# Optimization experiments

Hardware: AMD Instinct MI355X
Metric: run time of the kernel (lower is better)

Reference implementation:

```python
import jax, jax.numpy as jnp
import numpy as np

B, S, K_IN = 8, 2048, 512
D_MODEL = 1024
N_INPUT = 2048
N_PROCESS = 4096
HIDDEN = 4096  # default hidden_dim = n_input * 2
K = 256


def setup_inputs() -> dict:
    key = jax.random.key(0)
    ks = jax.random.split(key, 7)
    return {
        "selected_activations": jax.random.normal(ks[0], (B, S, K_IN), dtype=jnp.float32),
        "selected_indices": jax.random.randint(ks[1], (B, K_IN), 0, N_INPUT),
        "k": K,
        "combination_weights": jax.random.normal(ks[2], (N_PROCESS, N_INPUT), dtype=jnp.float32) * np.float32(np.sqrt(2.0 / N_INPUT)),
        "output_projections": jax.random.normal(ks[3], (N_PROCESS, D_MODEL), dtype=jnp.float32) * np.float32(np.sqrt(2.0 / N_PROCESS)),
        "w1": jax.random.normal(ks[4], (HIDDEN, N_INPUT), dtype=jnp.float32) * np.float32(np.sqrt(2.0 / (N_INPUT + HIDDEN))),
        "b1": jnp.zeros((HIDDEN,), dtype=jnp.float32),
        "w2": jax.random.normal(ks[5], (N_PROCESS, HIDDEN), dtype=jnp.float32) * np.float32(np.sqrt(2.0 / (HIDDEN + N_PROCESS))),
        "b2": jnp.zeros((N_PROCESS,), dtype=jnp.float32),
    }


def reference(selected_activations, selected_indices, k, combination_weights,
              output_projections, w1, b1, w2, b2):
    bsz = selected_indices.shape[0]
    n_input = combination_weights.shape[1]

    # Per-batch gather of combination weights: [B, k_in, n_process]
    sel_w = combination_weights.T[selected_indices]

    # Process activations: [B, S, n_process], exact (erf) GELU like torch F.gelu
    process_activations = jax.nn.gelu(
        jnp.einsum('bsk,bkp->bsp', selected_activations, sel_w), approximate=False)

    # One-hot style input-selection mask via scatter: [B, n_input]
    input_selection = jnp.zeros((bsz, n_input), dtype=jnp.float32)
    input_selection = input_selection.at[jnp.arange(bsz)[:, None], selected_indices].set(1.0)

    # Combination analyzer MLP: Linear -> GELU -> Linear
    h = jax.nn.gelu(input_selection @ w1.T + b1, approximate=False)
    combination_relevance = h @ w2.T + b2  # [B, n_process]

    # Router scores and top-k process selection
    activation_scores = process_activations.max(axis=1)  # [B, n_process]
    final_scores = activation_scores * jax.nn.sigmoid(combination_relevance)
    _, process_indices = jax.lax.top_k(final_scores, k)  # [B, k]

    # Gather selected process activations [B, S, k] and projections [B, k, d_model]
    sel_pa = jnp.take_along_axis(process_activations, process_indices[:, None, :], axis=2)
    sel_proj = output_projections[process_indices]

    # Final projection: [B, S, d_model]
    return jnp.einsum('bsk,bkd->bsd', sel_pa, sel_proj)
```

## Files before the change

kernel.cpp:

```cpp
#include <hip/hip_runtime.h>
#include <math.h>

#define B 8
#define S 2048
#define KIN 512
#define NIN 2048
#define NP 4096
#define HID 4096
#define DM 1024
#define TOPK 256

typedef __bf16 bf16x8 __attribute__((ext_vector_type(8)));
typedef __bf16 bf16x4 __attribute__((ext_vector_type(4)));
typedef float f32x4 __attribute__((ext_vector_type(4)));

__device__ __forceinline__ float gelu_exact(float x) {
    return 0.5f * x * (1.0f + erff(x * 0.70710678118654752440f));
}

__device__ __forceinline__ void atomicMaxFloat(float* addr, float val) {
    if (val >= 0.0f) atomicMax((int*)addr, __float_as_int(val));
    else             atomicMin((unsigned int*)addr, __float_as_uint(val));
}

__device__ __forceinline__ void async_copy16(void* lds, const void* g) {
    __builtin_amdgcn_global_load_lds(
        (__attribute__((address_space(1))) void*)g,
        (__attribute__((address_space(3))) void*)lds, 16, 0, 0);
}

__global__ __launch_bounds__(256) void init_kernel(float* scores, float* relacc,
                                                   float* hacc, unsigned* maskb,
                                                   int* selcnt) {
    int t = blockIdx.x * blockDim.x + threadIdx.x;
    if (t < B * NP)  { scores[t] = __int_as_float(0xFF800000); relacc[t] = 0.f; }
    if (t < B * HID) hacc[t] = 0.f;
    if (t < NIN)     maskb[t] = 0u;
    if (t < B)       selcnt[t] = 0;
}

__global__ __launch_bounds__(256) void scatter_maskbits(const int* __restrict__ idx,
                                                        unsigned* __restrict__ maskb) {
    int t = blockIdx.x * blockDim.x + threadIdx.x;
    if (t >= B * KIN) return;
    int b = t / KIN;
    atomicOr(&maskb[idx[t]], 1u << b);
}

__global__ __launch_bounds__(256) void pack_A(const float* __restrict__ A,
                                              __bf16* __restrict__ Apack) {
    size_t t = (size_t)blockIdx.x * 256 + threadIdx.x;
    size_t f = t * 4;
    size_t rowi = f >> 9;
    int j = (int)(f & 511);
    float4 v = *(const float4*)(A + f);
    __bf16 h0 = (__bf16)v.x, h1 = (__bf16)v.y, h2 = (__bf16)v.z, h3 = (__bf16)v.w;
    bf16x4 hv = {h0, h1, h2, h3};
    bf16x4 lv = {(__bf16)(v.x - (float)h0), (__bf16)(v.y - (float)h1),
                 (__bf16)(v.z - (float)h2), (__bf16)(v.w - (float)h3)};
    __bf16* orow = Apack + rowi * 1024;
    *(bf16x4*)(orow + j) = hv;
    *(bf16x4*)(orow + 512 + j) = lv;
}

__global__ __launch_bounds__(256) void gather_pack_w(const float* __restrict__ cw,
                                                     const int* __restrict__ idx,
                                                     __bf16* __restrict__ wpack) {
    __shared__ float rowbuf[4][NIN];
    __shared__ int sidx[B][KIN];
    int p0 = blockIdx.x * 4;
    int tid = threadIdx.x;
    for (int t = tid; t < B * KIN; t += 256) sidx[t >> 9][t & 511] = idx[t];
#pragma unroll
    for (int r = 0; r < 4; ++r)
        for (int c = tid; c < NIN / 4; c += 256)
            *(float4*)&rowbuf[r][c * 4] = *(const float4*)&cw[(size_t)(p0 + r) * NIN + c * 4];
    __syncthreads();
#pragma unroll
    for (int r = 0; r < 4; ++r) {
        int p = p0 + r;
        for (int b = 0; b < B; ++b) {
            __bf16* orow = wpack + ((size_t)b * NP + p) * 1024;
            for (int j = tid; j < KIN; j += 256) {
                float x = rowbuf[r][sidx[b][j]];
                __bf16 hh = (__bf16)x;
                orow[j] = hh;
                orow[512 + j] = (__bf16)(x - (float)hh);
            }
        }
    }
}

template <int EPI, int NSEG, int KSEG, int LDA, int LDB, int BROWS, int LDOUT>
__global__ __launch_bounds__(256) void mfma_gemm(const __bf16* __restrict__ Ap,
                                                 const __bf16* __restrict__ Bp,
                                                 void* __restrict__ outp) {
    __shared__ __align__(16) __bf16 As[128 * 64];
    __shared__ __align__(16) __bf16 Ws[128 * 64];
    const int b = blockIdx.z;
    const int s0 = blockIdx.x * 128;
    const int p0 = blockIdx.y * 128;
    const int tid = threadIdx.x;
    const int w = tid >> 6, lane = tid & 63;
    const int wr = w >> 1, wc = w & 1;
    const int ldRow = lane >> 3;
    const int ldCol = ((lane & 7) ^ (ldRow & 7)) * 8;
    const int fr = lane & 15;
    const int fq = lane >> 4;
    const __bf16* Ab = Ap + ((size_t)b * S + s0) * LDA;
    const __bf16* Bb = Bp + ((size_t)b * BROWS + p0) * LDB;

    f32x4 acc[4][4] = {};

    for (int seg = 0; seg < NSEG; ++seg) {
        const int aoff = (seg == 1) ? KSEG : 0;
        const int boff = (seg == 2) ? KSEG : 0;
        for (int k0 = 0; k0 < KSEG; k0 += 64) {
            __syncthreads();
#pragma unroll
            for (int i = 0; i < 4; ++i) {
                const __bf16* g = Ab + (size_t)(w * 32 + i * 8 + ldRow) * LDA + aoff + k0 + ldCol;
                async_copy16(&As[(w * 32 + i * 8) * 64], g);
            }
#pragma unroll
            for (int i = 0; i < 4; ++i) {
                const __bf16* g = Bb + (size_t)(w * 32 + i * 8 + ldRow) * LDB + boff + k0 + ldCol;
                async_copy16(&Ws[(w * 32 + i * 8) * 64], g);
            }
            __syncthreads();
#pragma unroll
            for (int ks = 0; ks < 2; ++ks) {
                bf16x8 af[4], bfr[4];
#pragma unroll
                for (int i = 0; i < 4; ++i) {
                    int R = wr * 64 + i * 16 + fr;
                    af[i] = *(const bf16x8*)&As[R * 64 + (((ks * 4 + fq) ^ (R & 7)) * 8)];
                }
#pragma unroll
                for (int j = 0; j < 4; ++j) {
                    int R = wc * 64 + j * 16 + fr;
                    bfr[j] = *(const bf16x8*)&Ws[R * 64 + (((ks * 4 + fq) ^ (R & 7)) * 8)];
                }
#pragma unroll
                for (int i = 0; i < 4; ++i)
#pragma unroll
                    for (int j = 0; j < 4; ++j)
                        acc[i][j] = __builtin_amdgcn_mfma_f32_16x16x32_bf16(af[i], bfr[j], acc[i][j], 0, 0, 0);
            }
        }
    }

    if constexpr (EPI == 1) {
        __bf16* o = (__bf16*)outp;
#pragma unroll
        for (int i = 0; i < 4; ++i)
#pragma unroll
            for (int r = 0; r < 4; ++r) {
                size_t row = (size_t)b * S + s0 + wr * 64 + i * 16 + fq * 4 + r;
#pragma unroll
                for (int j = 0; j < 4; ++j)
                    o[row * LDOUT + p0 + wc * 64 + j * 16 + fr] = (__bf16)gelu_exact(acc[i][j][r]);
            }
    } else {
        float* o = (float*)outp;
#pragma unroll
        for (int i = 0; i < 4; ++i)
#pragma unroll
            for (int r = 0; r < 4; ++r) {
                size_t row = (size_t)b * S + s0 + wr * 64 + i * 16 + fq * 4 + r;
#pragma unroll
                for (int j = 0; j < 4; ++j)
                    o[row * LDOUT + p0 + wc * 64 + j * 16 + fr] = acc[i][j][r];
            }
    }
}

__device__ __forceinline__ void stage64(__bf16* ldsTile, const __bf16* gRow0,
                                        int rbase, int ldg, int koff, int w, int lane) {
    const int rr = lane >> 3;
    const int gc = ((lane & 7) ^ rr) * 8;
    const __bf16* g = gRow0 + (size_t)(rbase + w * 8 + rr) * ldg + (koff + gc);
    async_copy16(ldsTile + (rbase + w * 8) * 64, g);
}

__device__ __forceinline__ void read_frags4(const __bf16* base, int row0, int fr,
                                            int fq, int kk, bf16x8* f) {
#pragma unroll
    for (int i = 0; i < 4; ++i) {
        int R = row0 + i * 16 + fr;
        f[i] = *(const bf16x8*)&base[R * 64 + (((kk * 4 + fq) ^ (R & 7)) * 8)];
    }
}

template <int EPI, int NSEG, int KSEG, int LDA, int LDB, int BROWS, int LDOUT>
__global__ __launch_bounds__(512, 2) void mfma_gemm256(const __bf16* __restrict__ Ap,
                                                       const __bf16* __restrict__ Bp,
                                                       void* __restrict__ outp) {
    constexpr int TPS = KSEG / 64;
    constexpr int NT = NSEG * TPS;
    __shared__ __align__(16) __bf16 As[2][256 * 64];
    __shared__ __align__(16) __bf16 Ws[2][256 * 64];
    const int b = blockIdx.z;
    const int s0 = blockIdx.x * 256;
    const int p0 = blockIdx.y * 256;
    const int tid = threadIdx.x;
    const int w = tid >> 6, lane = tid & 63;
    const int wr = w >> 2, wc = w & 3;
    const int fr = lane & 15, fq = lane >> 4;
    const __bf16* Ab = Ap + ((size_t)b * S + s0) * LDA;
    const __bf16* Bb = Bp + ((size_t)b * BROWS + p0) * LDB;

    auto offs = [&](int t, int& ao, int& bo) {
        int seg = t / TPS, k0 = (t % TPS) * 64;
        ao = ((NSEG == 3 && seg == 1) ? KSEG : 0) + k0;
        bo = ((NSEG == 3 && seg == 2) ? KSEG : 0) + k0;
    };

    f32x4 acc[8][4] = {};

    {
        int ao, bo;
        offs(0, ao, bo);
        stage64(&As[0][0], Ab, 0, LDA, ao, w, lane);
        stage64(&As[0][0], Ab, 128, LDA, ao, w, lane);
        stage64(&As[0][0], Ab, 64, LDA, ao, w, lane);
        stage64(&As[0][0], Ab, 192, LDA, ao, w, lane);
        stage64(&Ws[0][0], Bb, 0, LDB, bo, w, lane);
        stage64(&Ws[0][0], Bb, 128, LDB, bo, w, lane);
        stage64(&Ws[0][0], Bb, 64, LDB, bo, w, lane);
        stage64(&Ws[0][0], Bb, 192, LDB, bo, w, lane);
        if (NT > 1) {
            offs(1, ao, bo);
            stage64(&As[1][0], Ab, 0, LDA, ao, w, lane);
            stage64(&As[1][0], Ab, 128, LDA, ao, w, lane);
            stage64(&Ws[1][0], Bb, 0, LDB, bo, w, lane);
            stage64(&Ws[1][0], Bb, 128, LDB, bo, w, lane);
            asm volatile("s_waitcnt vmcnt(4)");
        } else {
            asm volatile("s_waitcnt vmcnt(0)");
        }
        __builtin_amdgcn_s_barrier();
    }

    for (int t = 0; t < NT; ++t) {
        __bf16* Asb = &As[t & 1][0];
        __bf16* Wsb = &Ws[t & 1][0];
        __bf16* Asn = &As[(t & 1) ^ 1][0];
        __bf16* Wsn = &Ws[(t & 1) ^ 1][0];
        bf16x8 af[4], bfr[4];

        read_frags4(Asb, wr * 128, fr, fq, 0, af);
        read_frags4(Wsb, wc * 64, fr, fq, 0, bfr);
        if (t + 1 < NT) {
            int ao, bo;
            offs(t + 1, ao, bo);
            stage64(Asn, Ab, 64, LDA, ao, w, lane);
            stage64(Asn, Ab, 192, LDA, ao, w, lane);
            stage64(Wsn, Bb, 64, LDB, bo, w, lane);
            stage64(Wsn, Bb, 192, LDB, bo, w, lane);
        }
        __builtin_amdgcn_s_barrier();
        asm volatile("s_waitcnt lgkmcnt(0)");
        __builtin_amdgcn_s_setprio(1);
#pragma unroll
        for (int mi = 0; mi < 4; ++mi)
#pragma unroll
            for (int nj = 0; nj < 4; ++nj)
                acc[mi][nj] = __builtin_amdgcn_mfma_f32_16x16x32_bf16(af[mi], bfr[nj], acc[mi][nj], 0, 0, 0);
        __builtin_amdgcn_s_setprio(0);
        __builtin_amdgcn_s_barrier();

        read_frags4(Asb, wr * 128 + 64, fr, fq, 0, af);
        __builtin_amdgcn_s_barrier();
        asm volatile("s_waitcnt lgkmcnt(0)");
        __builtin_amdgcn_s_setprio(1);
#pragma unroll
        for (int mi = 0; mi < 4; ++mi)
#pragma unroll
            for (int nj = 0; nj < 4; ++nj)
                acc[4 + mi][nj] = __builtin_amdgcn_mfma_f32_16x16x32_bf16(af[mi], bfr[nj], acc[4 + mi][nj], 0, 0, 0);
        __builtin_amdgcn_s_setprio(0);
        __builtin_amdgcn_s_barrier();

        read_frags4(Asb, wr * 128, fr, fq, 1, af);
        read_frags4(Wsb, wc * 64, fr, fq, 1, bfr);
        __builtin_amdgcn_s_barrier();
        asm volatile("s_waitcnt lgkmcnt(0)");
        __builtin_amdgcn_s_setprio(1);
#pragma unroll
        for (int mi = 0; mi < 4; ++mi)
#pragma unroll
            for (int nj = 0; nj < 4; ++nj)
                acc[mi][nj] = __builtin_amdgcn_mfma_f32_16x16x32_bf16(af[mi], bfr[nj], acc[mi][nj], 0, 0, 0);
        __builtin_amdgcn_s_setprio(0);
        __builtin_amdgcn_s_barrier();

        read_frags4(Asb, wr * 128 + 64, fr, fq, 1, af);
        if (t + 2 < NT) {
            int ao, bo;
            offs(t + 2, ao, bo);
            stage64(Asb, Ab, 0, LDA, ao, w, lane);
            stage64(Asb, Ab, 128, LDA, ao, w, lane);
            stage64(Wsb, Bb, 0, LDB, bo, w, lane);
            stage64(Wsb, Bb, 128, LDB, bo, w, lane);
            asm volatile("s_waitcnt vmcnt(4)");
        } else {
            asm volatile("s_waitcnt vmcnt(0)");
        }
        __builtin_amdgcn_s_barrier();
        asm volatile("s_waitcnt lgkmcnt(0)");
        __builtin_amdgcn_s_setprio(1);
#pragma unroll
        for (int mi = 0; mi < 4; ++mi)
#pragma unroll
            for (int nj = 0; nj < 4; ++nj)
                acc[4 + mi][nj] = __builtin_amdgcn_mfma_f32_16x16x32_bf16(af[mi], bfr[nj], acc[4 + mi][nj], 0, 0, 0);
        __builtin_amdgcn_s_setprio(0);
        __builtin_amdgcn_s_barrier();
    }

    if constexpr (EPI == 0) {
        float* scores = (float*)outp;
#pragma unroll
        for (int nj = 0; nj < 4; ++nj) {
            float mx = -INFINITY, mn = INFINITY;
#pragma unroll
            for (int mi = 0; mi < 8; ++mi)
#pragma unroll
                for (int r = 0; r < 4; ++r) {
                    float v = acc[mi][nj][r];
                    mx = fmaxf(mx, v);
                    mn = fminf(mn, v);
                }
            mx = fmaxf(mx, __shfl_xor(mx, 16));
            mx = fmaxf(mx, __shfl_xor(mx, 32));
            mn = fminf(mn, __shfl_xor(mn, 16));
            mn = fminf(mn, __shfl_xor(mn, 32));
            if (fq == 0) {
                float m = fmaxf(gelu_exact(mx), gelu_exact(mn));
                atomicMaxFloat(&scores[(size_t)b * LDOUT + p0 + wc * 64 + nj * 16 + fr], m);
            }
        }
    } else if constexpr (EPI == 1) {
        __bf16* o = (__bf16*)outp;
#pragma unroll
        for (int mi = 0; mi < 8; ++mi)
#pragma unroll
            for (int r = 0; r < 4; ++r) {
                size_t row = (size_t)b * S + s0 + wr * 128 + mi * 16 + fq * 4 + r;
#pragma unroll
                for (int nj = 0; nj < 4; ++nj)
                    o[row * LDOUT + p0 + wc * 64 + nj * 16 + fr] = (__bf16)gelu_exact(acc[mi][nj][r]);
            }
    } else {
        float* o = (float*)outp;
#pragma unroll
        for (int mi = 0; mi < 8; ++mi)
#pragma unroll
            for (int r = 0; r < 4; ++r) {
                size_t row = (size_t)b * S + s0 + wr * 128 + mi * 16 + fq * 4 + r;
#pragma unroll
                for (int nj = 0; nj < 4; ++nj)
                    o[row * LDOUT + p0 + wc * 64 + nj * 16 + fr] = acc[mi][nj][r];
            }
    }
}

__global__ __launch_bounds__(256) void mlp1_part(const float* __restrict__ w1,
                                                 const unsigned* __restrict__ maskb,
                                                 float* __restrict__ hacc) {
    __shared__ unsigned smb[512];
    int i0 = blockIdx.x * 64;
    int c0 = blockIdx.y * 512;
    int tid = threadIdx.x;
    for (int c = tid; c < 512; c += 256) smb[c] = maskb[c0 + c];
    __syncthreads();
    int r = tid >> 2, cq = tid & 3;
    const float* row = w1 + (size_t)(i0 + r) * NIN + c0;
    float acc[B] = {};
    for (int it = 0; it < 32; ++it) {
        int c = it * 16 + cq * 4;
        float4 v = *(const float4*)(row + c);
        float vv[4] = {v.x, v.y, v.z, v.w};
#pragma unroll
        for (int e = 0; e < 4; ++e) {
            unsigned mb = smb[c + e];
#pragma unroll
            for (int bb = 0; bb < B; ++bb)
                if (mb & (1u << bb)) acc[bb] += vv[e];
        }
    }
#pragma unroll
    for (int bb = 0; bb < B; ++bb)
        atomicAdd(&hacc[bb * HID + i0 + r], acc[bb]);
}

__global__ __launch_bounds__(256) void fin1(const float* __restrict__ hacc,
                                            const float* __restrict__ b1,
                                            float* __restrict__ h) {
    int t = blockIdx.x * 256 + threadIdx.x;
    if (t < B * HID) h[t] = gelu_exact(hacc[t] + b1[t & (HID - 1)]);
}

__global__ __launch_bounds__(256) void mlp2_part(const float* __restrict__ w2,
                                                 const float* __restrict__ h,
                                                 float* __restrict__ relacc) {
    __shared__ float sh[B][512];
    int p0 = blockIdx.x * 64;
    int c0 = blockIdx.y * 512;
    int tid = threadIdx.x;
    for (int i = tid; i < B * 128; i += 256) {
        int bb = i >> 7, c4 = i & 127;
        *(float4*)&sh[bb][c4 * 4] = *(const float4*)&h[(size_t)bb * HID + c0 + c4 * 4];
    }
    __syncthreads();
    int r = tid >> 2, cq = tid & 3;
    const float* row = w2 + (size_t)(p0 + r) * HID + c0;
    float acc[B] = {};
    for (int it = 0; it < 32; ++it) {
        int c = it * 16 + cq * 4;
        float4 v = *(const float4*)(row + c);
#pragma unroll
        for (int bb = 0; bb < B; ++bb)
            acc[bb] += v.x * sh[bb][c] + v.y * sh[bb][c + 1] + v.z * sh[bb][c + 2] + v.w * sh[bb][c + 3];
    }
#pragma unroll
    for (int bb = 0; bb < B; ++bb)
        atomicAdd(&relacc[bb * NP + p0 + r], acc[bb]);
}

__global__ __launch_bounds__(256) void fin2(const float* __restrict__ relacc,
                                            const float* __restrict__ b2,
                                            float* __restrict__ scores) {
    int t = blockIdx.x * 256 + threadIdx.x;
    if (t >= B * NP) return;
    float rel = relacc[t] + b2[t & (NP - 1)];
    scores[t] *= 1.0f / (1.0f + expf(-rel));
}

__global__ __launch_bounds__(256) void topk_select(const float* __restrict__ scores,
                                                   int* __restrict__ selidx,
                                                   int* __restrict__ selcnt) {
    __shared__ float sc[NP];
    int b = blockIdx.y;
    int p = blockIdx.x * 256 + threadIdx.x;
    for (int c = threadIdx.x; c < NP; c += 256) sc[c] = scores[(size_t)b * NP + c];
    __syncthreads();
    float my = sc[p];
    int cnt = 0;
    for (int q = 0; q < NP; ++q) {
        float v = sc[q];
        cnt += (v > my) || (v == my && q < p);
    }
    if (cnt < TOPK) {
        int pos = atomicAdd(&selcnt[b], 1);
        selidx[b * TOPK + pos] = p;
    }
}

__global__ __launch_bounds__(256) void wsel_gather(const __bf16* __restrict__ wpack,
                                                   const int* __restrict__ selidx,
                                                   __bf16* __restrict__ wsel) {
    int kk = blockIdx.x, b = blockIdx.y;
    int sel = selidx[b * TOPK + kk];
    const unsigned* src = (const unsigned*)(wpack + ((size_t)b * NP + sel) * 1024);
    unsigned* dst = (unsigned*)(wsel + ((size_t)b * TOPK + kk) * 512);
    dst[threadIdx.x] = src[threadIdx.x];
}

__global__ __launch_bounds__(256) void projT_gather(const float* __restrict__ proj,
                                                    const int* __restrict__ selidx,
                                                    __bf16* __restrict__ PT) {
    __shared__ float tile[64][68];
    __shared__ int sel[64];
    int b = blockIdx.z, d0 = blockIdx.x * 64, k0 = blockIdx.y * 64;
    int tid = threadIdx.x;
    if (tid < 64) sel[tid] = selidx[b * TOPK + k0 + tid];
    __syncthreads();
    for (int r = 0; r < 4; ++r) {
        int kk = r * 16 + (tid >> 4);
        float4 v = *(const float4*)&proj[(size_t)sel[kk] * DM + d0 + (tid & 15) * 4];
        *(float4*)&tile[kk][(tid & 15) * 4] = v;
    }
    __syncthreads();
    for (int r = 0; r < 16; ++r) {
        int dd = r * 4 + (tid >> 6);
        int kk = tid & 63;
        PT[((size_t)b * DM + d0 + dd) * TOPK + k0 + kk] = (__bf16)tile[kk][dd];
    }
}

extern "C" void kernel_launch(void* const* d_in, const int* in_sizes, int n_in,
                              void* d_out, int out_size, void* d_ws, size_t ws_size,
                              hipStream_t stream) {
    const float* A    = (const float*)d_in[0];
    const int*   idx  = (const int*)d_in[1];
    const float* cw   = (const float*)d_in[3];
    const float* proj = (const float*)d_in[4];
    const float* w1   = (const float*)d_in[5];
    const float* b1   = (const float*)d_in[6];
    const float* w2   = (const float*)d_in[7];
    const float* b2   = (const float*)d_in[8];
    float* out = (float*)d_out;

    char* ws = (char*)d_ws;
    size_t off = 0;
    auto alloc = [&](size_t bytes) {
        void* p = ws + off;
        off += (bytes + 255) & ~(size_t)255;
        return p;
    };
    __bf16* Apack = (__bf16*)alloc((size_t)B * S * 1024 * 2);
    __bf16* Wpack = (__bf16*)alloc((size_t)B * NP * 1024 * 2);
    __bf16* selpa = (__bf16*)alloc((size_t)B * S * TOPK * 2);
    __bf16* PT    = (__bf16*)alloc((size_t)B * DM * TOPK * 2);
    __bf16* Wsel  = (__bf16*)alloc((size_t)B * TOPK * 512 * 2);
    float* scores = (float*)alloc((size_t)B * NP * 4);
    float* relacc = (float*)alloc((size_t)B * NP * 4);
    float* hacc   = (float*)alloc((size_t)B * HID * 4);
    float* h      = (float*)alloc((size_t)B * HID * 4);
    unsigned* maskb = (unsigned*)alloc((size_t)NIN * 4);
    int* selidx   = (int*)alloc((size_t)B * TOPK * 4);
    int* selcnt   = (int*)alloc((size_t)B * 4);

    init_kernel<<<dim3((B * HID + 255) / 256), 256, 0, stream>>>(scores, relacc, hacc, maskb, selcnt);
    scatter_maskbits<<<dim3((B * KIN + 255) / 256), 256, 0, stream>>>(idx, maskb);
    pack_A<<<dim3((B * S * KIN / 4) / 256), 256, 0, stream>>>(A, Apack);
    gather_pack_w<<<dim3(NP / 4), 256, 0, stream>>>(cw, idx, Wpack);

    mfma_gemm256<0, 3, 512, 1024, 1024, NP, NP>
        <<<dim3(S / 256, NP / 256, B), 512, 0, stream>>>(Apack, Wpack, (void*)scores);

    mlp1_part<<<dim3(HID / 64, NIN / 512), 256, 0, stream>>>(w1, maskb, hacc);
    fin1<<<dim3((B * HID + 255) / 256), 256, 0, stream>>>(hacc, b1, h);
    mlp2_part<<<dim3(NP / 64, HID / 512), 256, 0, stream>>>(w2, h, relacc);
    fin2<<<dim3((B * NP + 255) / 256), 256, 0, stream>>>(relacc, b2, scores);

    topk_select<<<dim3(NP / 256, B), 256, 0, stream>>>(scores, selidx, selcnt);

    wsel_gather<<<dim3(TOPK, B), 256, 0, stream>>>(Wpack, selidx, Wsel);
    projT_gather<<<dim3(DM / 64, TOPK / 64, B), 256, 0, stream>>>(proj, selidx, PT);

    mfma_gemm<1, 1, 512, 1024, 512, TOPK, TOPK>
        <<<dim3(S / 128, TOPK / 128, B), 256, 0, stream>>>(Apack, Wsel, (void*)selpa);

    mfma_gemm<2, 1, 256, 256, 256, DM, DM>
        <<<dim3(S / 128, DM / 128, B), 256, 0, stream>>>(selpa, PT, (void*)out);
}
```

Measured before the change: 682.6 us.

## Fuse sigmoid scoring into top-k, remap GEMM blocks batch-fastest, precompute LDS offsets

Removes the separate fin2 kernel by computing the sigmoid-weighted scores while loading them into shared memory in topk_select, saving one launch and a global read/write pass. The big scoring GEMM now maps its flat block index so that consecutive blocks walk across batches first, which changes which tiles run concurrently and how they share cache. Swizzled LDS fragment offsets are precomputed once into registers instead of recomputed each iteration, which may raise register pressure. The top-k kernel now recomputes the sigmoid redundantly in each of its blocks per batch.

```diff
diff --git a/kernel.cpp b/kernel.cpp
--- a/kernel.cpp
+++ b/kernel.cpp
@@ -183,15 +183,6 @@
     async_copy16(ldsTile + (rbase + w * 8) * 64, g);
 }
 
-__device__ __forceinline__ void read_frags4(const __bf16* base, int row0, int fr,
-                                            int fq, int kk, bf16x8* f) {
-#pragma unroll
-    for (int i = 0; i < 4; ++i) {
-        int R = row0 + i * 16 + fr;
-        f[i] = *(const bf16x8*)&base[R * 64 + (((kk * 4 + fq) ^ (R & 7)) * 8)];
-    }
-}
-
 template <int EPI, int NSEG, int KSEG, int LDA, int LDB, int BROWS, int LDOUT>
 __global__ __launch_bounds__(512, 2) void mfma_gemm256(const __bf16* __restrict__ Ap,
                                                        const __bf16* __restrict__ Bp,
@@ -200,9 +191,13 @@
     constexpr int NT = NSEG * TPS;
     __shared__ __align__(16) __bf16 As[2][256 * 64];
     __shared__ __align__(16) __bf16 Ws[2][256 * 64];
-    const int b = blockIdx.z;
-    const int s0 = blockIdx.x * 256;
-    const int p0 = blockIdx.y * 256;
+
+    const int flat = blockIdx.x + (blockIdx.y << 3) + (blockIdx.z << 7);
+    const int b = flat & 7;
+    const int j = flat >> 3;
+    const int s0 = (j & 7) * 256;
+    const int p0 = (j >> 3) * 256;
+
     const int tid = threadIdx.x;
     const int w = tid >> 6, lane = tid & 63;
     const int wr = w >> 2, wc = w & 3;
@@ -215,6 +210,24 @@
         ao = ((NSEG == 3 && seg == 1) ? KSEG : 0) + k0;
         bo = ((NSEG == 3 && seg == 2) ? KSEG : 0) + k0;
     };
+
+    int offA[2][2][4];
+    int offB[2][4];
+#pragma unroll
+    for (int kk = 0; kk < 2; ++kk) {
+#pragma unroll
+        for (int mh = 0; mh < 2; ++mh)
+#pragma unroll
+            for (int mi = 0; mi < 4; ++mi) {
+                int R = wr * 128 + mh * 64 + mi * 16 + fr;
+                offA[kk][mh][mi] = R * 64 + (((kk * 4 + fq) ^ (R & 7)) * 8);
+            }
+#pragma unroll
+        for (int nj = 0; nj < 4; ++nj) {
+            int R = wc * 64 + nj * 16 + fr;
+            offB[kk][nj] = R * 64 + (((kk * 4 + fq) ^ (R & 7)) * 8);
+        }
+    }
 
     f32x4 acc[8][4] = {};
 
@@ -243,14 +256,16 @@
     }
 
     for (int t = 0; t < NT; ++t) {
-        __bf16* Asb = &As[t & 1][0];
-        __bf16* Wsb = &Ws[t & 1][0];
+        const __bf16* Asb = &As[t & 1][0];
+        const __bf16* Wsb = &Ws[t & 1][0];
         __bf16* Asn = &As[(t & 1) ^ 1][0];
         __bf16* Wsn = &Ws[(t & 1) ^ 1][0];
         bf16x8 af[4], bfr[4];
 
-        read_frags4(Asb, wr * 128, fr, fq, 0, af);
-        read_frags4(Wsb, wc * 64, fr, fq, 0, bfr);
+#pragma unroll
+        for (int i = 0; i < 4; ++i) af[i] = *(const bf16x8*)&Asb[offA[0][0][i]];
+#pragma unroll
+        for (int n = 0; n < 4; ++n) bfr[n] = *(const bf16x8*)&Wsb[offB[0][n]];
         if (t + 1 < NT) {
             int ao, bo;
             offs(t + 1, ao, bo);
@@ -270,7 +285,8 @@
         __builtin_amdgcn_s_setprio(0);
         __builtin_amdgcn_s_barrier();
 
-        read_frags4(Asb, wr * 128 + 64, fr, fq, 0, af);
+#pragma unroll
+        for (int i = 0; i < 4; ++i) af[i] = *(const bf16x8*)&Asb[offA[0][1][i]];
         __builtin_amdgcn_s_barrier();
         asm volatile("s_waitcnt lgkmcnt(0)");
         __builtin_amdgcn_s_setprio(1);
@@ -282,8 +298,10 @@
         __builtin_amdgcn_s_setprio(0);
         __builtin_amdgcn_s_barrier();
 
-        read_frags4(Asb, wr * 128, fr, fq, 1, af);
-        read_frags4(Wsb, wc * 64, fr, fq, 1, bfr);
+#pragma unroll
+        for (int i = 0; i < 4; ++i) af[i] = *(const bf16x8*)&Asb[offA[1][0][i]];
+#pragma unroll
+        for (int n = 0; n < 4; ++n) bfr[n] = *(const bf16x8*)&Wsb[offB[1][n]];
         __builtin_amdgcn_s_barrier();
         asm volatile("s_waitcnt lgkmcnt(0)");
         __builtin_amdgcn_s_setprio(1);
@@ -295,14 +313,15 @@
         __builtin_amdgcn_s_setprio(0);
         __builtin_amdgcn_s_barrier();
 
-        read_frags4(Asb, wr * 128 + 64, fr, fq, 1, af);
+#pragma unroll
+        for (int i = 0; i < 4; ++i) af[i] = *(const bf16x8*)&Asb[offA[1][1][i]];
         if (t + 2 < NT) {
             int ao, bo;
             offs(t + 2, ao, bo);
-            stage64(Asb, Ab, 0, LDA, ao, w, lane);
-            stage64(Asb, Ab, 128, LDA, ao, w, lane);
-            stage64(Wsb, Bb, 0, LDB, bo, w, lane);
-            stage64(Wsb, Bb, 128, LDB, bo, w, lane);
+            stage64((__bf16*)Asb, Ab, 0, LDA, ao, w, lane);
+            stage64((__bf16*)Asb, Ab, 128, LDA, ao, w, lane);
+            stage64((__bf16*)Wsb, Bb, 0, LDB, bo, w, lane);
+            stage64((__bf16*)Wsb, Bb, 128, LDB, bo, w, lane);
             asm volatile("s_waitcnt vmcnt(4)");
         } else {
             asm volatile("s_waitcnt vmcnt(0)");
@@ -429,22 +448,18 @@
         atomicAdd(&relacc[bb * NP + p0 + r], acc[bb]);
 }
 
-__global__ __launch_bounds__(256) void fin2(const float* __restrict__ relacc,
-                                            const float* __restrict__ b2,
-                                            float* __restrict__ scores) {
-    int t = blockIdx.x * 256 + threadIdx.x;
-    if (t >= B * NP) return;
-    float rel = relacc[t] + b2[t & (NP - 1)];
-    scores[t] *= 1.0f / (1.0f + expf(-rel));
-}
-
 __global__ __launch_bounds__(256) void topk_select(const float* __restrict__ scores,
+                                                   const float* __restrict__ relacc,
+                                                   const float* __restrict__ b2,
                                                    int* __restrict__ selidx,
                                                    int* __restrict__ selcnt) {
     __shared__ float sc[NP];
     int b = blockIdx.y;
     int p = blockIdx.x * 256 + threadIdx.x;
-    for (int c = threadIdx.x; c < NP; c += 256) sc[c] = scores[(size_t)b * NP + c];
+    for (int c = threadIdx.x; c < NP; c += 256) {
+        float rel = relacc[(size_t)b * NP + c] + b2[c];
+        sc[c] = scores[(size_t)b * NP + c] * (1.0f / (1.0f + expf(-rel)));
+    }
     __syncthreads();
     float my = sc[p];
     int cnt = 0;
@@ -534,9 +549,8 @@
     mlp1_part<<<dim3(HID / 64, NIN / 512), 256, 0, stream>>>(w1, maskb, hacc);
     fin1<<<dim3((B * HID + 255) / 256), 256, 0, stream>>>(hacc, b1, h);
     mlp2_part<<<dim3(NP / 64, HID / 512), 256, 0, stream>>>(w2, h, relacc);
-    fin2<<<dim3((B * NP + 255) / 256), 256, 0, stream>>>(relacc, b2, scores);
-
-    topk_select<<<dim3(NP / 256, B), 256, 0, stream>>>(scores, selidx, selcnt);
+
+    topk_select<<<dim3(NP / 256, B), 256, 0, stream>>>(scores, relacc, b2, selidx, selcnt);
 
     wsel_gather<<<dim3(TOPK, B), 256, 0, stream>>>(Wpack, selidx, Wsel);
     projT_gather<<<dim3(DM / 64, TOPK / 64, B), 256, 0, stream>>>(proj, selidx, PT);
```

Result: no change. 672.7 us (-1.4%).
